# Kernel optimization log

Measured on AMD Instinct MI355X. Metric: run time of the kernel, lower is better.

The kernel has to match this reference:

```python
import jax, jax.numpy as jnp
import numpy as np

B, D, O, E = 8192, 1024, 1024, 8

def setup_inputs() -> dict:
    key = jax.random.key(0)
    ks = jax.random.split(key, 5)
    s = 1.0 / np.sqrt(D)
    return {
        "x": jax.random.normal(ks[0], (B, D), dtype=jnp.float32),
        "Wg": jax.random.uniform(ks[1], (D, E), jnp.float32, -s, s),
        "bg": jax.random.uniform(ks[2], (E,), jnp.float32, -s, s),
        "We": jax.random.uniform(ks[3], (E, D, O), jnp.float32, -s, s),
        "be": jax.random.uniform(ks[4], (E, O), jnp.float32, -s, s),
    }

def reference(x, Wg, bg, We, be):
    # gating: [B, E], softmax over experts (dim=1)
    gates = jax.nn.softmax(x @ Wg + bg, axis=1)
    # dense expert outputs: [B, E, O] (single batched GEMM over all experts)
    expert_out = jnp.einsum('bd,edo->beo', x, We) + be[None, :, :]
    # softmax-weighted combine (bmm of [B,1,E] @ [B,E,O] -> [B,O])
    return jnp.einsum('be,beo->bo', gates, expert_out)
```

## Files before the change

kernel.cpp:

```cpp
#include <hip/hip_runtime.h>
#include <hip/hip_bf16.h>
#include <stdint.h>

#define B_SZ 8192
#define D_SZ 1024
#define O_SZ 1024
#define E_SZ 8

#define BM 256
#define BN 128
#define BK 64
#define NT 128

typedef __bf16 bf16_t;
typedef __bf16 bf16x8 __attribute__((ext_vector_type(8)));
typedef __bf16 bf16x4 __attribute__((ext_vector_type(4)));
typedef float  f32x4  __attribute__((ext_vector_type(4)));

__global__ __launch_bounds__(256) void gating_cvt_kernel(
    const float* __restrict__ x, const float* __restrict__ Wg,
    const float* __restrict__ bg, float* __restrict__ gates,
    bf16_t* __restrict__ xb) {
  const int w = threadIdx.x >> 6, lane = threadIdx.x & 63;
  const int b = blockIdx.x * 4 + w;
  const float4* xr = (const float4*)(x + (size_t)b * D_SZ);
  bf16x4* xbr = (bf16x4*)(xb + (size_t)b * D_SZ);
  float acc[8];
#pragma unroll
  for (int e = 0; e < 8; ++e) acc[e] = 0.f;
#pragma unroll 1
  for (int it = 0; it < 4; ++it) {
    int d4 = it * 64 + lane;
    float4 v = xr[d4];
    bf16x4 ob;
    ob[0] = (bf16_t)v.x; ob[1] = (bf16_t)v.y;
    ob[2] = (bf16_t)v.z; ob[3] = (bf16_t)v.w;
    xbr[d4] = ob;
    const float4* wr = (const float4*)(Wg + (size_t)d4 * 32);
    float xs[4] = {v.x, v.y, v.z, v.w};
#pragma unroll
    for (int rr = 0; rr < 4; ++rr) {
      float4 wa = wr[rr * 2], wb = wr[rr * 2 + 1];
      acc[0] += xs[rr] * wa.x; acc[1] += xs[rr] * wa.y;
      acc[2] += xs[rr] * wa.z; acc[3] += xs[rr] * wa.w;
      acc[4] += xs[rr] * wb.x; acc[5] += xs[rr] * wb.y;
      acc[6] += xs[rr] * wb.z; acc[7] += xs[rr] * wb.w;
    }
  }
#pragma unroll
  for (int off = 32; off >= 1; off >>= 1) {
#pragma unroll
    for (int e = 0; e < 8; ++e) acc[e] += __shfl_xor(acc[e], off, 64);
  }
  if (lane == 0) {
#pragma unroll
    for (int e = 0; e < 8; ++e) acc[e] += bg[e];
    float m = acc[0];
#pragma unroll
    for (int e = 1; e < 8; ++e) m = fmaxf(m, acc[e]);
    float s = 0.f, ex[8];
#pragma unroll
    for (int e = 0; e < 8; ++e) { ex[e] = __expf(acc[e] - m); s += ex[e]; }
    float inv = 1.0f / s;
    float* gr = gates + (size_t)b * 8;
#pragma unroll
    for (int e = 0; e < 8; ++e) gr[e] = ex[e] * inv;
  }
}

__global__ __launch_bounds__(256) void transpose_we(
    const float* __restrict__ We, bf16_t* __restrict__ WeT) {
  __shared__ float tile[64][65];
  const int e = blockIdx.z;
  const int d0 = blockIdx.y * 64, o0 = blockIdx.x * 64;
  const int tx = threadIdx.x & 63, ty = threadIdx.x >> 6;
  const float* src = We + (size_t)e * D_SZ * O_SZ;
#pragma unroll
  for (int i = 0; i < 16; ++i) {
    int d = ty + i * 4;
    tile[d][tx] = src[(size_t)(d0 + d) * O_SZ + o0 + tx];
  }
  __syncthreads();
  bf16_t* dst = WeT + (size_t)e * O_SZ * D_SZ;
#pragma unroll
  for (int i = 0; i < 16; ++i) {
    int o = ty + i * 4;
    dst[(size_t)(o0 + o) * D_SZ + d0 + tx] = (bf16_t)tile[tx][o];
  }
}

__device__ __forceinline__ void gl16(const bf16_t* g, const bf16_t* l) {
  __builtin_amdgcn_global_load_lds(
      (const __attribute__((address_space(1))) void*)g,
      (__attribute__((address_space(3))) void*)l, 16, 0, 0);
}

__global__ __launch_bounds__(512, 2) void moe_gemm(
    const bf16_t* __restrict__ xb,
    const bf16_t* __restrict__ wet,
    const float* __restrict__ gates,
    const float* __restrict__ be,
    float* __restrict__ out)
{
  __shared__ bf16_t lA[3][BM * BK];
  __shared__ bf16_t lB[3][BN * BK];
  __shared__ float  lG[BM * 9];
  __shared__ float  lBe[E_SZ * BN];

  const int tid = threadIdx.x;
  const int w = tid >> 6, lane = tid & 63;

  const int flat = blockIdx.x + (blockIdx.y << 3);
  const int xcd = flat & 7, slot = flat >> 3;
  const int bt = (xcd << 2) + (slot & 3);
  const int ot = slot >> 2;
  const int b0 = bt * BM;
  const int o0 = ot * BN;

  const int wm = (w >> 1) * 64, wn = (w & 1) * 64;
  const int m16 = lane & 15, q = lane >> 4;

  {
    float4 g4 = ((const float4*)(gates + (size_t)b0 * 8))[tid];
    int gr = tid >> 1, gc = (tid & 1) * 4;
    lG[gr * 9 + gc + 0] = g4.x; lG[gr * 9 + gc + 1] = g4.y;
    lG[gr * 9 + gc + 2] = g4.z; lG[gr * 9 + gc + 3] = g4.w;
#pragma unroll
    for (int p = 0; p < 2; ++p) {
      int idx = tid + p * 512;
      lBe[idx] = be[(size_t)(idx >> 7) * O_SZ + o0 + (idx & 127)];
    }
  }

  const bf16_t* aptr[4]; int aoffL[4];
#pragma unroll
  for (int j = 0; j < 4; ++j) {
    int g0 = w * 64 + 512 * j;
    int row = (g0 >> 3) + (lane >> 3);
    int ls = (lane & 7) ^ (row & 7);
    aptr[j] = xb + (size_t)(b0 + row) * D_SZ + ls * 8;
    aoffL[j] = g0 * 8;
  }
  const bf16_t* bptr[2]; int boffL[2];
#pragma unroll
  for (int j = 0; j < 2; ++j) {
    int g0 = w * 64 + 512 * j;
    int row = (g0 >> 3) + (lane >> 3);
    int ls = (lane & 7) ^ (row & 7);
    bptr[j] = wet + (size_t)(o0 + row) * D_SZ + ls * 8;
    boffL[j] = g0 * 8;
  }

#define STAGE(t_, buf_) do {                                                   \
    const int kk_ = ((t_) & 15) << 6;                                          \
    const size_t eo_ = (((size_t)((t_) >> 4)) << 20) + kk_;                    \
    _Pragma("unroll")                                                          \
    for (int js = 0; js < 4; ++js) gl16(aptr[js] + kk_, &lA[buf_][0] + aoffL[js]); \
    _Pragma("unroll")                                                          \
    for (int js = 0; js < 2; ++js) gl16(bptr[js] + eo_, &lB[buf_][0] + boffL[js]); \
  } while (0)

  f32x4 acc[4][4], outAcc[4][4];
#pragma unroll
  for (int i = 0; i < 4; ++i)
#pragma unroll
    for (int j = 0; j < 4; ++j) {
      acc[i][j] = f32x4{0.f, 0.f, 0.f, 0.f};
      outAcc[i][j] = f32x4{0.f, 0.f, 0.f, 0.f};
    }

  STAGE(0, 0);
  STAGE(1, 1);
  asm volatile("s_waitcnt lgkmcnt(0)" ::: "memory");

#define BODY(cur_) do {                                                        \
    const bf16_t* la_ = &lA[cur_][0];                                          \
    const bf16_t* lb_ = &lB[cur_][0];                                          \
    bf16x8 bfr[4][2];                                                          \
    _Pragma("unroll")                                                          \
    for (int j = 0; j < 4; ++j) {                                              \
      int r = wn + j * 16 + m16;                                               \
      const char* rb = (const char*)lb_ + r * 128;                             \
      bfr[j][0] = *(const bf16x8*)(rb + (((q) ^ (r & 7)) << 4));               \
      bfr[j][1] = *(const bf16x8*)(rb + (((4 | q) ^ (r & 7)) << 4));           \
    }                                                                          \
    _Pragma("unroll")                                                          \
    for (int i = 0; i < 4; ++i) {                                              \
      int r = wm + i * 16 + m16;                                               \
      const char* ra = (const char*)la_ + r * 128;                             \
      bf16x8 a0 = *(const bf16x8*)(ra + (((q) ^ (r & 7)) << 4));               \
      bf16x8 a1 = *(const bf16x8*)(ra + (((4 | q) ^ (r & 7)) << 4));           \
      _Pragma("unroll")                                                        \
      for (int j = 0; j < 4; ++j) {                                            \
        acc[i][j] = __builtin_amdgcn_mfma_f32_16x16x32_bf16(                   \
            a0, bfr[j][0], acc[i][j], 0, 0, 0);                                \
        acc[i][j] = __builtin_amdgcn_mfma_f32_16x16x32_bf16(                   \
            a1, bfr[j][1], acc[i][j], 0, 0, 0);                                \
      }                                                                        \
    }                                                                          \
  } while (0)

#define COMBINE(e_) do {                                                       \
    float bec_[4];                                                             \
    _Pragma("unroll")                                                          \
    for (int j = 0; j < 4; ++j) bec_[j] = lBe[(e_) * BN + wn + j * 16 + m16];  \
    _Pragma("unroll")                                                          \
    for (int i = 0; i < 4; ++i) {                                              \
      _Pragma("unroll")                                                        \
      for (int rg = 0; rg < 4; ++rg) {                                         \
        float gv = lG[(wm + i * 16 + q * 4 + rg) * 9 + (e_)];                  \
        _Pragma("unroll")                                                      \
        for (int j = 0; j < 4; ++j) {                                          \
          outAcc[i][j][rg] += gv * (acc[i][j][rg] + bec_[j]);                  \
          acc[i][j][rg] = 0.f;                                                 \
        }                                                                      \
      }                                                                        \
    }                                                                          \
  } while (0)

  int cur = 0;
#pragma unroll 1
  for (int t = 0; t < NT - 1; ++t) {
    asm volatile("s_waitcnt vmcnt(6)" ::: "memory");
    __builtin_amdgcn_s_barrier();
    asm volatile("" ::: "memory");
    if (t <= NT - 3) {
      int nb = cur + 2; if (nb >= 3) nb -= 3;
      STAGE(t + 2, nb);
    }
    BODY(cur);
    if ((t & 15) == 15) COMBINE(t >> 4);
    ++cur; if (cur == 3) cur = 0;
  }
  asm volatile("s_waitcnt vmcnt(0)" ::: "memory");
  __builtin_amdgcn_s_barrier();
  asm volatile("" ::: "memory");
  BODY(cur);
  COMBINE(7);

#pragma unroll
  for (int i = 0; i < 4; ++i)
#pragma unroll
    for (int rg = 0; rg < 4; ++rg) {
      float* orow = out + (size_t)(b0 + wm + i * 16 + q * 4 + rg) * O_SZ
                    + o0 + wn + m16;
#pragma unroll
      for (int j = 0; j < 4; ++j) orow[j * 16] = outAcc[i][j][rg];
    }
}

extern "C" void kernel_launch(void* const* d_in, const int* in_sizes, int n_in,
                              void* d_out, int out_size, void* d_ws, size_t ws_size,
                              hipStream_t stream) {
  const float* x  = (const float*)d_in[0];
  const float* Wg = (const float*)d_in[1];
  const float* bg = (const float*)d_in[2];
  const float* We = (const float*)d_in[3];
  const float* be = (const float*)d_in[4];
  float* out = (float*)d_out;

  char* ws = (char*)d_ws;
  float*  gates = (float*)ws;
  bf16_t* xb    = (bf16_t*)(ws + (1 << 18));
  bf16_t* wet   = (bf16_t*)(ws + (1 << 18) + (1 << 24));

  gating_cvt_kernel<<<B_SZ / 4, 256, 0, stream>>>(x, Wg, bg, gates, xb);
  transpose_we<<<dim3(O_SZ / 64, D_SZ / 64, E_SZ), 256, 0, stream>>>(We, wet);
  moe_gemm<<<dim3(O_SZ / BN, B_SZ / BM), 512, 0, stream>>>(xb, wet, gates, be, out);
}
```

Baseline: 292.2 us.

## Merge prep kernels, unroll GEMM pipeline by three, precompute LDS offsets with setprio

The gating/convert and weight-transpose kernels are merged into one launch, with block-index ranges selecting the role. This removes a launch and lets the two prep phases run concurrently. The GEMM main loop is unrolled by three so buffer indices are compile-time constants and the per-iteration guard disappears. LDS fragment offsets are precomputed, and each BODY is split into two half-K phases wrapped in s_setprio so MFMAs get priority. The tail handling is restructured, and the larger unrolled body raises register pressure and code size.

```diff
diff --git a/kernel.cpp b/kernel.cpp
--- a/kernel.cpp
+++ b/kernel.cpp
@@ -17,75 +17,77 @@
 typedef __bf16 bf16x4 __attribute__((ext_vector_type(4)));
 typedef float  f32x4  __attribute__((ext_vector_type(4)));
 
-__global__ __launch_bounds__(256) void gating_cvt_kernel(
+__global__ __launch_bounds__(256) void prep_kernel(
     const float* __restrict__ x, const float* __restrict__ Wg,
-    const float* __restrict__ bg, float* __restrict__ gates,
-    bf16_t* __restrict__ xb) {
-  const int w = threadIdx.x >> 6, lane = threadIdx.x & 63;
-  const int b = blockIdx.x * 4 + w;
-  const float4* xr = (const float4*)(x + (size_t)b * D_SZ);
-  bf16x4* xbr = (bf16x4*)(xb + (size_t)b * D_SZ);
-  float acc[8];
-#pragma unroll
-  for (int e = 0; e < 8; ++e) acc[e] = 0.f;
+    const float* __restrict__ bg, const float* __restrict__ We,
+    float* __restrict__ gates, bf16_t* __restrict__ xb,
+    bf16_t* __restrict__ wet) {
+  __shared__ float tile[64][65];
+  const int bid = blockIdx.x;
+  if (bid < 2048) {
+    const int w = threadIdx.x >> 6, lane = threadIdx.x & 63;
+    const int b = bid * 4 + w;
+    const float4* xr = (const float4*)(x + (size_t)b * D_SZ);
+    bf16x4* xbr = (bf16x4*)(xb + (size_t)b * D_SZ);
+    float acc[8];
+#pragma unroll
+    for (int e = 0; e < 8; ++e) acc[e] = 0.f;
 #pragma unroll 1
-  for (int it = 0; it < 4; ++it) {
-    int d4 = it * 64 + lane;
-    float4 v = xr[d4];
-    bf16x4 ob;
-    ob[0] = (bf16_t)v.x; ob[1] = (bf16_t)v.y;
-    ob[2] = (bf16_t)v.z; ob[3] = (bf16_t)v.w;
-    xbr[d4] = ob;
-    const float4* wr = (const float4*)(Wg + (size_t)d4 * 32);
-    float xs[4] = {v.x, v.y, v.z, v.w};
-#pragma unroll
-    for (int rr = 0; rr < 4; ++rr) {
-      float4 wa = wr[rr * 2], wb = wr[rr * 2 + 1];
-      acc[0] += xs[rr] * wa.x; acc[1] += xs[rr] * wa.y;
-      acc[2] += xs[rr] * wa.z; acc[3] += xs[rr] * wa.w;
-      acc[4] += xs[rr] * wb.x; acc[5] += xs[rr] * wb.y;
-      acc[6] += xs[rr] * wb.z; acc[7] += xs[rr] * wb.w;
-    }
-  }
-#pragma unroll
-  for (int off = 32; off >= 1; off >>= 1) {
-#pragma unroll
-    for (int e = 0; e < 8; ++e) acc[e] += __shfl_xor(acc[e], off, 64);
-  }
-  if (lane == 0) {
-#pragma unroll
-    for (int e = 0; e < 8; ++e) acc[e] += bg[e];
-    float m = acc[0];
-#pragma unroll
-    for (int e = 1; e < 8; ++e) m = fmaxf(m, acc[e]);
-    float s = 0.f, ex[8];
-#pragma unroll
-    for (int e = 0; e < 8; ++e) { ex[e] = __expf(acc[e] - m); s += ex[e]; }
-    float inv = 1.0f / s;
-    float* gr = gates + (size_t)b * 8;
-#pragma unroll
-    for (int e = 0; e < 8; ++e) gr[e] = ex[e] * inv;
-  }
-}
-
-__global__ __launch_bounds__(256) void transpose_we(
-    const float* __restrict__ We, bf16_t* __restrict__ WeT) {
-  __shared__ float tile[64][65];
-  const int e = blockIdx.z;
-  const int d0 = blockIdx.y * 64, o0 = blockIdx.x * 64;
-  const int tx = threadIdx.x & 63, ty = threadIdx.x >> 6;
-  const float* src = We + (size_t)e * D_SZ * O_SZ;
-#pragma unroll
-  for (int i = 0; i < 16; ++i) {
-    int d = ty + i * 4;
-    tile[d][tx] = src[(size_t)(d0 + d) * O_SZ + o0 + tx];
-  }
-  __syncthreads();
-  bf16_t* dst = WeT + (size_t)e * O_SZ * D_SZ;
-#pragma unroll
-  for (int i = 0; i < 16; ++i) {
-    int o = ty + i * 4;
-    dst[(size_t)(o0 + o) * D_SZ + d0 + tx] = (bf16_t)tile[tx][o];
+    for (int it = 0; it < 4; ++it) {
+      int d4 = it * 64 + lane;
+      float4 v = xr[d4];
+      bf16x4 ob;
+      ob[0] = (bf16_t)v.x; ob[1] = (bf16_t)v.y;
+      ob[2] = (bf16_t)v.z; ob[3] = (bf16_t)v.w;
+      xbr[d4] = ob;
+      const float4* wr = (const float4*)(Wg + (size_t)d4 * 32);
+      float xs[4] = {v.x, v.y, v.z, v.w};
+#pragma unroll
+      for (int rr = 0; rr < 4; ++rr) {
+        float4 wa = wr[rr * 2], wb = wr[rr * 2 + 1];
+        acc[0] += xs[rr] * wa.x; acc[1] += xs[rr] * wa.y;
+        acc[2] += xs[rr] * wa.z; acc[3] += xs[rr] * wa.w;
+        acc[4] += xs[rr] * wb.x; acc[5] += xs[rr] * wb.y;
+        acc[6] += xs[rr] * wb.z; acc[7] += xs[rr] * wb.w;
+      }
+    }
+#pragma unroll
+    for (int off = 32; off >= 1; off >>= 1) {
+#pragma unroll
+      for (int e = 0; e < 8; ++e) acc[e] += __shfl_xor(acc[e], off, 64);
+    }
+    if (lane == 0) {
+#pragma unroll
+      for (int e = 0; e < 8; ++e) acc[e] += bg[e];
+      float m = acc[0];
+#pragma unroll
+      for (int e = 1; e < 8; ++e) m = fmaxf(m, acc[e]);
+      float s = 0.f, ex[8];
+#pragma unroll
+      for (int e = 0; e < 8; ++e) { ex[e] = __expf(acc[e] - m); s += ex[e]; }
+      float inv = 1.0f / s;
+      float* gr = gates + (size_t)b * 8;
+#pragma unroll
+      for (int e = 0; e < 8; ++e) gr[e] = ex[e] * inv;
+    }
+  } else {
+    const int bt = bid - 2048;
+    const int e = bt >> 8;
+    const int d0 = ((bt >> 4) & 15) * 64, o0 = (bt & 15) * 64;
+    const int tx = threadIdx.x & 63, ty = threadIdx.x >> 6;
+    const float* src = We + (size_t)e * D_SZ * O_SZ;
+#pragma unroll
+    for (int i = 0; i < 16; ++i) {
+      int d = ty + i * 4;
+      tile[d][tx] = src[(size_t)(d0 + d) * O_SZ + o0 + tx];
+    }
+    __syncthreads();
+    bf16_t* dst = wet + (size_t)e * O_SZ * D_SZ;
+#pragma unroll
+    for (int i = 0; i < 16; ++i) {
+      int o = ty + i * 4;
+      dst[(size_t)(o0 + o) * D_SZ + d0 + tx] = (bf16_t)tile[tx][o];
+    }
   }
 }
 
@@ -151,6 +153,12 @@
     boffL[j] = g0 * 8;
   }
 
+  const int xk = m16 & 7;
+  const int offA0 = (wm + m16) * 128 + ((q ^ xk) << 4);
+  const int offA1 = (wm + m16) * 128 + (((4 | q) ^ xk) << 4);
+  const int offB0 = (wn + m16) * 128 + ((q ^ xk) << 4);
+  const int offB1 = (wn + m16) * 128 + (((4 | q) ^ xk) << 4);
+
 #define STAGE(t_, buf_) do {                                                   \
     const int kk_ = ((t_) & 15) << 6;                                          \
     const size_t eo_ = (((size_t)((t_) >> 4)) << 20) + kk_;                    \
@@ -174,30 +182,33 @@
   asm volatile("s_waitcnt lgkmcnt(0)" ::: "memory");
 
 #define BODY(cur_) do {                                                        \
-    const bf16_t* la_ = &lA[cur_][0];                                          \
-    const bf16_t* lb_ = &lB[cur_][0];                                          \
-    bf16x8 bfr[4][2];                                                          \
-    _Pragma("unroll")                                                          \
-    for (int j = 0; j < 4; ++j) {                                              \
-      int r = wn + j * 16 + m16;                                               \
-      const char* rb = (const char*)lb_ + r * 128;                             \
-      bfr[j][0] = *(const bf16x8*)(rb + (((q) ^ (r & 7)) << 4));               \
-      bfr[j][1] = *(const bf16x8*)(rb + (((4 | q) ^ (r & 7)) << 4));           \
-    }                                                                          \
-    _Pragma("unroll")                                                          \
-    for (int i = 0; i < 4; ++i) {                                              \
-      int r = wm + i * 16 + m16;                                               \
-      const char* ra = (const char*)la_ + r * 128;                             \
-      bf16x8 a0 = *(const bf16x8*)(ra + (((q) ^ (r & 7)) << 4));               \
-      bf16x8 a1 = *(const bf16x8*)(ra + (((4 | q) ^ (r & 7)) << 4));           \
+    const char* la_ = (const char*)(&lA[cur_][0]);                             \
+    const char* lb_ = (const char*)(&lB[cur_][0]);                             \
+    bf16x8 a_[4], b_[4];                                                       \
+    _Pragma("unroll")                                                          \
+    for (int j = 0; j < 4; ++j) b_[j] = *(const bf16x8*)(lb_ + offB0 + j * 2048); \
+    _Pragma("unroll")                                                          \
+    for (int i = 0; i < 4; ++i) a_[i] = *(const bf16x8*)(la_ + offA0 + i * 2048); \
+    __builtin_amdgcn_s_setprio(1);                                             \
+    _Pragma("unroll")                                                          \
+    for (int i = 0; i < 4; ++i)                                                \
       _Pragma("unroll")                                                        \
-      for (int j = 0; j < 4; ++j) {                                            \
+      for (int j = 0; j < 4; ++j)                                              \
         acc[i][j] = __builtin_amdgcn_mfma_f32_16x16x32_bf16(                   \
-            a0, bfr[j][0], acc[i][j], 0, 0, 0);                                \
+            a_[i], b_[j], acc[i][j], 0, 0, 0);                                 \
+    __builtin_amdgcn_s_setprio(0);                                             \
+    _Pragma("unroll")                                                          \
+    for (int j = 0; j < 4; ++j) b_[j] = *(const bf16x8*)(lb_ + offB1 + j * 2048); \
+    _Pragma("unroll")                                                          \
+    for (int i = 0; i < 4; ++i) a_[i] = *(const bf16x8*)(la_ + offA1 + i * 2048); \
+    __builtin_amdgcn_s_setprio(1);                                             \
+    _Pragma("unroll")                                                          \
+    for (int i = 0; i < 4; ++i)                                                \
+      _Pragma("unroll")                                                        \
+      for (int j = 0; j < 4; ++j)                                              \
         acc[i][j] = __builtin_amdgcn_mfma_f32_16x16x32_bf16(                   \
-            a1, bfr[j][1], acc[i][j], 0, 0, 0);                                \
-      }                                                                        \
-    }                                                                          \
+            a_[i], b_[j], acc[i][j], 0, 0, 0);                                 \
+    __builtin_amdgcn_s_setprio(0);                                             \
   } while (0)
 
 #define COMBINE(e_) do {                                                       \
@@ -218,24 +229,29 @@
     }                                                                          \
   } while (0)
 
-  int cur = 0;
+#define STEP_S(t_, cur_, nb_) do {                                             \
+    asm volatile("s_waitcnt vmcnt(6)" ::: "memory");                           \
+    __builtin_amdgcn_s_barrier();                                              \
+    asm volatile("" ::: "memory");                                             \
+    STAGE((t_) + 2, nb_);                                                      \
+    BODY(cur_);                                                                \
+    if (((t_) & 15) == 15) COMBINE((t_) >> 4);                                 \
+  } while (0)
+
 #pragma unroll 1
-  for (int t = 0; t < NT - 1; ++t) {
-    asm volatile("s_waitcnt vmcnt(6)" ::: "memory");
-    __builtin_amdgcn_s_barrier();
-    asm volatile("" ::: "memory");
-    if (t <= NT - 3) {
-      int nb = cur + 2; if (nb >= 3) nb -= 3;
-      STAGE(t + 2, nb);
-    }
-    BODY(cur);
-    if ((t & 15) == 15) COMBINE(t >> 4);
-    ++cur; if (cur == 3) cur = 0;
-  }
+  for (int t3 = 0; t3 < 126; t3 += 3) {
+    STEP_S(t3 + 0, 0, 2);
+    STEP_S(t3 + 1, 1, 0);
+    STEP_S(t3 + 2, 2, 1);
+  }
+  asm volatile("s_waitcnt vmcnt(6)" ::: "memory");
+  __builtin_amdgcn_s_barrier();
+  asm volatile("" ::: "memory");
+  BODY(0);
   asm volatile("s_waitcnt vmcnt(0)" ::: "memory");
   __builtin_amdgcn_s_barrier();
   asm volatile("" ::: "memory");
-  BODY(cur);
+  BODY(1);
   COMBINE(7);
 
 #pragma unroll
@@ -264,7 +280,6 @@
   bf16_t* xb    = (bf16_t*)(ws + (1 << 18));
   bf16_t* wet   = (bf16_t*)(ws + (1 << 18) + (1 << 24));
 
-  gating_cvt_kernel<<<B_SZ / 4, 256, 0, stream>>>(x, Wg, bg, gates, xb);
-  transpose_we<<<dim3(O_SZ / 64, D_SZ / 64, E_SZ), 256, 0, stream>>>(We, wet);
+  prep_kernel<<<4096, 256, 0, stream>>>(x, Wg, bg, We, gates, xb, wet);
   moe_gemm<<<dim3(O_SZ / BN, B_SZ / BM), 512, 0, stream>>>(xb, wet, gates, be, out);
 }
```

Measured after the change: 256.9 us. 12.1% less time.
